# Kernel optimization log

Hardware: AMD Instinct MI355X
Metric: run time of the kernel (lower is better)

Reference implementation:

```python
import jax, jax.numpy as jnp
import numpy as np

IN, H, OUT, T, B = 132, 1024, 132, 100, 256


def setup_inputs() -> dict:
    key = jax.random.key(0)
    ks = jax.random.split(key, 16)
    s_in = 1.0 / np.sqrt(H)
    def mk(k, shape):
        return jax.random.uniform(k, shape, jnp.float32, -s_in, s_in)
    inp = {
        "real_seq": jax.random.normal(ks[0], (B, T, IN), jnp.float32),
        "W_ih1": mk(ks[1], (4 * H, IN)), "W_hh1": mk(ks[2], (4 * H, H)),
        "b_ih1": mk(ks[3], (4 * H,)),   "b_hh1": mk(ks[4], (4 * H,)),
        "W_ih2": mk(ks[5], (4 * H, H)), "W_hh2": mk(ks[6], (4 * H, H)),
        "b_ih2": mk(ks[7], (4 * H,)),   "b_hh2": mk(ks[8], (4 * H,)),
        "W_ih3": mk(ks[9], (4 * H, H)), "W_hh3": mk(ks[10], (4 * H, H)),
        "b_ih3": mk(ks[11], (4 * H,)),  "b_hh3": mk(ks[12], (4 * H,)),
        "W_dec": mk(ks[13], (OUT, H)),  "b_dec": mk(ks[14], (OUT,)),
        "condition_num": 5, "groundtruth_num": 5,
    }
    return inp


def _lstm_cell(x, h, c, W_ih, W_hh, b_ih, b_hh):
    # torch LSTMCell: gates in (i, f, g, o) order
    gates = x @ W_ih.T + b_ih + h @ W_hh.T + b_hh
    i, f, g, o = jnp.split(gates, 4, axis=-1)
    i, f, o = jax.nn.sigmoid(i), jax.nn.sigmoid(f), jax.nn.sigmoid(o)
    g = jnp.tanh(g)
    c_new = f * c + i * g
    h_new = o * jnp.tanh(c_new)
    return h_new, c_new


def reference(real_seq, W_ih1, W_hh1, b_ih1, b_hh1,
              W_ih2, W_hh2, b_ih2, b_hh2,
              W_ih3, W_hh3, b_ih3, b_hh3,
              W_dec, b_dec, condition_num, groundtruth_num):
    batch, seq_len, _ = real_seq.shape
    # static teacher-forcing schedule: [1]*gt_num + [0]*cond_num, tiled
    gt = np.ones((100, groundtruth_num)); con = np.zeros((100, condition_num))
    cond = jnp.asarray(np.concatenate((gt, con), 1).reshape(-1)[:seq_len] == 1)

    z = jnp.zeros((batch, H), jnp.float32)
    init = (z, z, z, z, z, z, jnp.zeros((batch, OUT), jnp.float32))

    def step(carry, xs):
        h0, h1, h2, c0, c1, c2, prev_out = carry
        frame, use_gt = xs
        x = jnp.where(use_gt, frame, prev_out)
        # note: lstm2/lstm3 consume the OLD h0/h1, faithful to forward_lstm
        nh0, nc0 = _lstm_cell(x,  h0, c0, W_ih1, W_hh1, b_ih1, b_hh1)
        nh1, nc1 = _lstm_cell(h0, h1, c1, W_ih2, W_hh2, b_ih2, b_hh2)
        nh2, nc2 = _lstm_cell(h1, h2, c2, W_ih3, W_hh3, b_ih3, b_hh3)
        out = nh2 @ W_dec.T + b_dec
        return (nh0, nh1, nh2, nc0, nc1, nc2, out), out

    xs = (jnp.swapaxes(real_seq, 0, 1), cond)  # [T,B,IN], [T]
    _, outs = jax.lax.scan(step, init, xs)      # outs: [T,B,OUT]
    # torch concatenates along dim 1 each step -> [B, T*OUT]
    return jnp.swapaxes(outs, 0, 1).reshape(batch, seq_len * OUT)
```

## Files before the change

kernel.cpp:

```cpp
#include <hip/hip_runtime.h>
#include <math.h>

#define B_   256
#define T_   100
#define IN_  132
#define OUT_ 132
#define H_   1024
#define BH   ((size_t)B_ * H_)
#define WSZ  ((size_t)4096 * H_)

typedef _Float16 f16;
typedef _Float16 f16x8 __attribute__((ext_vector_type(8)));
typedef float    f32x4 __attribute__((ext_vector_type(4)));

#define MFMA16(a, b, c) __builtin_amdgcn_mfma_f32_16x16x32_f16((a), (b), (c), 0, 0, 0)

#define AS1 __attribute__((address_space(1)))
#define AS3 __attribute__((address_space(3)))

__device__ __forceinline__ void gl_lds16(const void* g, void* l) {
    __builtin_amdgcn_global_load_lds((AS1 void*)g, (AS3 void*)l, 16, 0, 0);
}

__device__ __forceinline__ float sigmoidf_(float x) {
    return 1.0f / (1.0f + __expf(-x));
}
__device__ __forceinline__ float tanhf_(float x) {
    float e = __expf(2.0f * x);
    return 1.0f - 2.0f / (e + 1.0f);
}


__global__ void conv_pad(const float* __restrict__ src, f16* __restrict__ dst,
                         int src_rows, int src_k, int dst_k) {
    int k = blockIdx.x * 256 + threadIdx.x;
    int r = blockIdx.y;
    if (k >= dst_k) return;
    float v = (r < src_rows && k < src_k) ? src[(size_t)r * src_k + k] : 0.0f;
    dst[(size_t)r * dst_k + k] = (f16)v;
}

__global__ void convT_kernel(const float* __restrict__ Wd, f16* __restrict__ WdT) {
    int k = blockIdx.x * 256 + threadIdx.x;
    int m = blockIdx.y;
    if (k >= 160) return;
    float v = (k < IN_) ? Wd[(size_t)k * H_ + m] : 0.0f;
    WdT[(size_t)m * 160 + k] = (f16)v;
}

__global__ void bias_add_kernel(const float* __restrict__ a, const float* __restrict__ b,
                                float* __restrict__ dst, int n) {
    int i = blockIdx.x * 256 + threadIdx.x;
    if (i < n) dst[i] = a[i] + b[i];
}

__global__ void bfb_kernel(const float* __restrict__ Wih1, const float* __restrict__ bd,
                           float* __restrict__ bfb) {
    int j = blockIdx.x * 256 + threadIdx.x;
    if (j >= 4096) return;
    float s = 0.0f;
    for (int k = 0; k < IN_; ++k) s += Wih1[(size_t)j * IN_ + k] * bd[k];
    bfb[j] = s;
}

__global__ void zero_kernel(float* __restrict__ p, int n) {
    int i = blockIdx.x * blockDim.x + threadIdx.x;
    int st = gridDim.x * blockDim.x;
    for (; i < n; i += st) p[i] = 0.0f;
}

__global__ __launch_bounds__(256) void wfb_mfma(
    const f16* __restrict__ W0, const f16* __restrict__ WdT, f16* __restrict__ Wfb)
{
    const int m0 = blockIdx.x * 128;
    const int n0 = blockIdx.y * 128;
    const int tid  = threadIdx.x;
    const int lane = tid & 63;
    const int w    = tid >> 6;
    const int lx   = lane & 15;
    const int quad = lane >> 4;
    const int wrow = w >> 1, wcol = w & 1;

    __shared__ __align__(16) char lds[32768];

    auto stA = [&](int kt, int buf) {
        char* base = lds + buf * 16384;
#pragma unroll
        for (int i = 0; i < 2; ++i) {
            int r  = w * 32 + i * 16 + (lane >> 2);
            int sg = (lane & 3) ^ (r & 3);
            const f16* g = W0 + (size_t)(m0 + r) * 160 + kt * 32 + sg * 8;
            gl_lds16(g, base + (size_t)(w * 32 + i * 16) * 64);
        }
    };
    auto stB = [&](int kt, int buf) {
        char* base = lds + 8192 + buf * 16384;
#pragma unroll
        for (int i = 0; i < 2; ++i) {
            int r  = w * 32 + i * 16 + (lane >> 2);
            int sg = (lane & 3) ^ (r & 3);
            const f16* g = WdT + (size_t)(n0 + r) * 160 + kt * 32 + sg * 8;
            gl_lds16(g, base + (size_t)(w * 32 + i * 16) * 64);
        }
    };

    f32x4 acc[4][4];
#pragma unroll
    for (int m = 0; m < 4; ++m)
#pragma unroll
        for (int n = 0; n < 4; ++n) acc[m][n] = (f32x4){0.f, 0.f, 0.f, 0.f};

    stA(0, 0); stB(0, 0);
    for (int kt = 0; kt < 5; ++kt) {
        __syncthreads();
        if (kt + 1 < 5) { stA(kt + 1, (kt + 1) & 1); stB(kt + 1, (kt + 1) & 1); }
        const char* bA = lds + (kt & 1) * 16384;
        const char* bB = lds + 8192 + (kt & 1) * 16384;
        f16x8 af[4], bf[4];
#pragma unroll
        for (int m = 0; m < 4; ++m) {
            int R = wrow * 64 + m * 16 + lx;
            af[m] = *(const f16x8*)(bA + R * 64 + ((quad ^ (R & 3)) * 16));
        }
#pragma unroll
        for (int n = 0; n < 4; ++n) {
            int R = wcol * 64 + n * 16 + lx;
            bf[n] = *(const f16x8*)(bB + R * 64 + ((quad ^ (R & 3)) * 16));
        }
#pragma unroll
        for (int m = 0; m < 4; ++m)
#pragma unroll
            for (int n = 0; n < 4; ++n)
                acc[m][n] = MFMA16(af[m], bf[n], acc[m][n]);
    }

#pragma unroll
    for (int m = 0; m < 4; ++m)
#pragma unroll
        for (int n = 0; n < 4; ++n)
#pragma unroll
            for (int r = 0; r < 4; ++r) {
                int row = m0 + wrow * 64 + m * 16 + quad * 4 + r;
                int col = n0 + wcol * 64 + n * 16 + lx;
                Wfb[(size_t)row * H_ + col] = (f16)acc[m][n][r];
            }
}

__global__ __launch_bounds__(256) void step_mfma(
    const float* __restrict__ seq,
    const f16* __restrict__ hfb,
    const f16* __restrict__ h2old,
    const f16* __restrict__ h01c,
    f16* __restrict__ h01n,
    f16* __restrict__ h2out,
    float* __restrict__ c_st,
    const f16* __restrict__ W0,
    const f16* __restrict__ Wb,
    const f16* __restrict__ Wfb,
    const float* __restrict__ bias_comb,
    const float* __restrict__ bfb,
    const int* __restrict__ cnum, const int* __restrict__ gnum,
    int t)
{
    const int j0   = blockIdx.x * 32;
    const int mb   = blockIdx.y;
    const int l    = blockIdx.z;
    const int tid  = threadIdx.x;
    const int lane = tid & 63;
    const int w    = tid >> 6;
    const int lx   = lane & 15;
    const int quad = lane >> 4;
    const int wrow = w >> 1, wcol = w & 1;

    __shared__ __align__(16) char lds[24576];

    bool use_gt = false, seqmode = false;
    int n0 = 32, ldk0 = H_;
    const f16 *Ap0 = nullptr, *Wp0 = nullptr;
    if (l == 0) {
        int cn = cnum[0], gn = gnum[0];
        use_gt = (t % (cn + gn)) < gn;
        if (use_gt)      { seqmode = true; Wp0 = W0; ldk0 = 160; n0 = 5; }
        else if (t == 0) { n0 = 0; }
        else             { Ap0 = hfb; Wp0 = Wfb; }
    } else if (l == 1) { Ap0 = h01c;      Wp0 = Wb + 1 * WSZ; }
    else               { Ap0 = h01c + BH; Wp0 = Wb + 3 * WSZ; }
    const f16* Ap1 = (l == 0) ? h01c : (l == 1) ? (h01c + BH) : h2old;
    const f16* Wp1 = Wb + (size_t)((l == 0) ? 0 : (l == 1) ? 2 : 4) * WSZ;
    const int ntot = n0 + 32;

    auto stA = [&](const f16* Ap, int kk, int buf) {
        char* base = lds + buf * 12288 + w * 1024;
        int row = w * 16 + (lane >> 2);
        int sg  = (lane & 3) ^ (row & 3);
        const f16* g = Ap + (size_t)(mb * 64 + row) * H_ + kk * 32 + sg * 8;
        gl_lds16(g, base);
    };
    auto stAseq = [&](int kk, int buf) {
        char* base = lds + buf * 12288;
        int rl = tid >> 2, sl = tid & 3;
        int sg = sl ^ (rl & 3);
        int b  = mb * 64 + rl;
        f16x8 vv;
#pragma unroll
        for (int e = 0; e < 8; ++e) {
            int k = kk * 32 + sg * 8 + e;
            float v = (k < IN_) ? seq[((size_t)b * T_ + t) * IN_ + k] : 0.0f;
            vv[e] = (f16)v;
        }
        *(f16x8*)(base + rl * 64 + sl * 16) = vv;
    };
    auto stB = [&](const f16* Wp, size_t ldk, int kk, int buf) {
        char* base = lds + 4096 + buf * 12288;
#pragma unroll
        for (int i = 0; i < 2; ++i) {
            int c    = w * 32 + i * 16 + (lane >> 2);
            int sg   = (lane & 3) ^ (c & 3);
            int gate = (c >> 4) & 3;
            int jj   = (c & 15) + (c >> 6) * 16;
            const f16* g = Wp + (size_t)(gate * H_ + j0 + jj) * ldk + kk * 32 + sg * 8;
            gl_lds16(g, base + (size_t)(w * 32 + i * 16) * 64);
        }
    };
    auto stage = [&](int kt, int buf) {
        if (kt < n0) {
            if (seqmode) stAseq(kt, buf); else stA(Ap0, kt, buf);
            stB(Wp0, (size_t)ldk0, kt, buf);
        } else {
            stA(Ap1, kt - n0, buf);
            stB(Wp1, (size_t)H_, kt - n0, buf);
        }
    };

    f32x4 acc[2][4];
#pragma unroll
    for (int m = 0; m < 2; ++m)
#pragma unroll
        for (int n = 0; n < 4; ++n) acc[m][n] = (f32x4){0.f, 0.f, 0.f, 0.f};

    stage(0, 0);
    for (int kt = 0; kt < ntot; ++kt) {
        __syncthreads();
        if (kt + 1 < ntot) stage(kt + 1, (kt + 1) & 1);
        const char* bA = lds + (kt & 1) * 12288;
        const char* bB = lds + 4096 + (kt & 1) * 12288;
        f16x8 af[2], bf[4];
#pragma unroll
        for (int m = 0; m < 2; ++m) {
            int R = wrow * 32 + m * 16 + lx;
            af[m] = *(const f16x8*)(bA + R * 64 + ((quad ^ (R & 3)) * 16));
        }
#pragma unroll
        for (int n = 0; n < 4; ++n) {
            int R = wcol * 64 + n * 16 + lx;
            bf[n] = *(const f16x8*)(bB + R * 64 + ((quad ^ (R & 3)) * 16));
        }
#pragma unroll
        for (int m = 0; m < 2; ++m)
#pragma unroll
            for (int n = 0; n < 4; ++n)
                acc[m][n] = MFMA16(af[m], bf[n], acc[m][n]);
    }

    const int j = j0 + wcol * 16 + lx;
    const float* bc = bias_comb + l * 4096;
    const bool addfb = (l == 0 && !use_gt && t > 0);
    float bi  = bc[j]        + (addfb ? bfb[j]        : 0.f);
    float bff = bc[1024 + j] + (addfb ? bfb[1024 + j] : 0.f);
    float bg  = bc[2048 + j] + (addfb ? bfb[2048 + j] : 0.f);
    float bo  = bc[3072 + j] + (addfb ? bfb[3072 + j] : 0.f);
#pragma unroll
    for (int m = 0; m < 2; ++m) {
#pragma unroll
        for (int r = 0; r < 4; ++r) {
            int b = mb * 64 + wrow * 32 + m * 16 + quad * 4 + r;
            float gi = acc[m][0][r] + bi;
            float gf = acc[m][1][r] + bff;
            float gg = acc[m][2][r] + bg;
            float go = acc[m][3][r] + bo;
            size_t ix = ((size_t)l * B_ + b) * H_ + j;
            float cn = sigmoidf_(gf) * c_st[ix] + sigmoidf_(gi) * tanhf_(gg);
            c_st[ix] = cn;
            float hv = sigmoidf_(go) * tanhf_(cn);
            if (l == 2) h2out[(size_t)b * H_ + j] = (f16)hv;
            else        h01n[(size_t)l * BH + (size_t)b * H_ + j] = (f16)hv;
        }
    }
}

__global__ __launch_bounds__(256) void decode_mfma(
    const f16* __restrict__ hist,
    const f16* __restrict__ Wd16,
    const float* __restrict__ bd,
    float* __restrict__ dout)
{
    const int r0  = blockIdx.x * 128;
    const int nb0 = blockIdx.y * 32;
    const int tid  = threadIdx.x;
    const int lane = tid & 63;
    const int w    = tid >> 6;
    const int lx   = lane & 15;
    const int quad = lane >> 4;

    __shared__ __align__(16) char lds[20480];

    auto stA = [&](int kt, int buf) {
        char* base = lds + buf * 10240;
#pragma unroll
        for (int i = 0; i < 2; ++i) {
            int r  = w * 32 + i * 16 + (lane >> 2);
            int sg = (lane & 3) ^ (r & 3);
            const f16* g = hist + (size_t)(r0 + r) * H_ + kt * 32 + sg * 8;
            gl_lds16(g, base + (size_t)(w * 32 + i * 16) * 64);
        }
    };
    auto stB = [&](int kt, int buf) {
        char* base = lds + 8192 + buf * 10240;
        if (w < 2) {
            int r  = w * 16 + (lane >> 2);
            int sg = (lane & 3) ^ (r & 3);
            const f16* g = Wd16 + (size_t)(nb0 + r) * H_ + kt * 32 + sg * 8;
            gl_lds16(g, base + (size_t)(w * 16) * 64);
        }
    };

    f32x4 acc[2][2];
#pragma unroll
    for (int m = 0; m < 2; ++m)
#pragma unroll
        for (int n = 0; n < 2; ++n) acc[m][n] = (f32x4){0.f, 0.f, 0.f, 0.f};

    stA(0, 0); stB(0, 0);
    for (int kt = 0; kt < 32; ++kt) {
        __syncthreads();
        if (kt + 1 < 32) { stA(kt + 1, (kt + 1) & 1); stB(kt + 1, (kt + 1) & 1); }
        const char* bA = lds + (kt & 1) * 10240;
        const char* bB = lds + 8192 + (kt & 1) * 10240;
        f16x8 af[2], bf[2];
#pragma unroll
        for (int m = 0; m < 2; ++m) {
            int R = w * 32 + m * 16 + lx;
            af[m] = *(const f16x8*)(bA + R * 64 + ((quad ^ (R & 3)) * 16));
        }
#pragma unroll
        for (int n = 0; n < 2; ++n) {
            int R = n * 16 + lx;
            bf[n] = *(const f16x8*)(bB + R * 64 + ((quad ^ (R & 3)) * 16));
        }
#pragma unroll
        for (int m = 0; m < 2; ++m)
#pragma unroll
            for (int n = 0; n < 2; ++n)
                acc[m][n] = MFMA16(af[m], bf[n], acc[m][n]);
    }

#pragma unroll
    for (int n = 0; n < 2; ++n) {
        int nn = nb0 + n * 16 + lx;
        if (nn < OUT_) {
            float bv = bd[nn];
#pragma unroll
            for (int m = 0; m < 2; ++m)
#pragma unroll
                for (int r = 0; r < 4; ++r) {
                    int row = r0 + w * 32 + m * 16 + quad * 4 + r;
                    int tt = row >> 8, b = row & 255;
                    dout[(size_t)b * (T_ * OUT_) + (size_t)tt * OUT_ + nn] = acc[m][n][r] + bv;
                }
        }
    }
}


extern "C" void kernel_launch(void* const* d_in, const int* in_sizes, int n_in,
                              void* d_out, int out_size, void* d_ws, size_t ws_size,
                              hipStream_t stream) {
    const float* seq  = (const float*)d_in[0];
    const float* Wih1 = (const float*)d_in[1];
    const float* Whh1 = (const float*)d_in[2];
    const float* bih1 = (const float*)d_in[3];
    const float* bhh1 = (const float*)d_in[4];
    const float* Wih2 = (const float*)d_in[5];
    const float* Whh2 = (const float*)d_in[6];
    const float* bih2 = (const float*)d_in[7];
    const float* bhh2 = (const float*)d_in[8];
    const float* Wih3 = (const float*)d_in[9];
    const float* Whh3 = (const float*)d_in[10];
    const float* bih3 = (const float*)d_in[11];
    const float* bhh3 = (const float*)d_in[12];
    const float* Wd   = (const float*)d_in[13];
    const float* bd   = (const float*)d_in[14];
    const int*   cnum = (const int*)d_in[15];
    const int*   gnum = (const int*)d_in[16];

    char* p = (char*)d_ws;
    f16*  W0   = (f16*)p;  p += (size_t)4096 * 160 * 2;
    f16*  Wb   = (f16*)p;  p += (size_t)5 * 4096 * 1024 * 2;
    f16*  Wd16 = (f16*)p;  p += (size_t)160 * 1024 * 2;
    f16*  WdT  = (f16*)p;  p += (size_t)1024 * 160 * 2;
    f16*  Wfb  = (f16*)p;  p += (size_t)4096 * 1024 * 2;
    float* bias_comb = (float*)p; p += (size_t)3 * 4096 * 4;
    float* bfb = (float*)p; p += (size_t)4096 * 4;
    f16*  hist = (f16*)p;  p += (size_t)100 * BH * 2;
    f16*  h01a = (f16*)p;  p += (size_t)2 * BH * 2;
    f16*  h01b = (f16*)p;  p += (size_t)2 * BH * 2;
    float* c_st = (float*)p; p += (size_t)3 * BH * 4;
    const int zero_floats = (int)(((size_t)4 * BH * 2 + (size_t)3 * BH * 4) / 4);

    conv_pad<<<dim3(1, 4096), 256, 0, stream>>>(Wih1, W0, 4096, IN_, 160);
    conv_pad<<<dim3(4, 4096), 256, 0, stream>>>(Whh1, Wb + 0 * WSZ, 4096, H_, H_);
    conv_pad<<<dim3(4, 4096), 256, 0, stream>>>(Wih2, Wb + 1 * WSZ, 4096, H_, H_);
    conv_pad<<<dim3(4, 4096), 256, 0, stream>>>(Whh2, Wb + 2 * WSZ, 4096, H_, H_);
    conv_pad<<<dim3(4, 4096), 256, 0, stream>>>(Wih3, Wb + 3 * WSZ, 4096, H_, H_);
    conv_pad<<<dim3(4, 4096), 256, 0, stream>>>(Whh3, Wb + 4 * WSZ, 4096, H_, H_);
    conv_pad<<<dim3(4, 160), 256, 0, stream>>>(Wd, Wd16, OUT_, H_, H_);
    convT_kernel<<<dim3(1, 1024), 256, 0, stream>>>(Wd, WdT);
    bias_add_kernel<<<16, 256, 0, stream>>>(bih1, bhh1, bias_comb + 0 * 4096, 4096);
    bias_add_kernel<<<16, 256, 0, stream>>>(bih2, bhh2, bias_comb + 1 * 4096, 4096);
    bias_add_kernel<<<16, 256, 0, stream>>>(bih3, bhh3, bias_comb + 2 * 4096, 4096);
    bfb_kernel<<<16, 256, 0, stream>>>(Wih1, bd, bfb);
    wfb_mfma<<<dim3(32, 8), 256, 0, stream>>>(W0, WdT, Wfb);
    zero_kernel<<<512, 256, 0, stream>>>((float*)h01a, zero_floats);

    f16 *hc = h01a, *hn = h01b;
    for (int t = 0; t < T_; ++t) {
        const f16* hfb   = (t > 0) ? (hist + (size_t)(t - 1) * BH) : hc;
        const f16* h2old = (t > 0) ? (hist + (size_t)(t - 1) * BH) : hc;
        step_mfma<<<dim3(32, 4, 3), 256, 0, stream>>>(
            seq, hfb, h2old, hc, hn, hist + (size_t)t * BH, c_st,
            W0, Wb, Wfb, bias_comb, bfb, cnum, gnum, t);
        f16* tmp = hc; hc = hn; hn = tmp;
    }

    decode_mfma<<<dim3(200, 5), 256, 0, stream>>>(hist, Wd16, bd, (float*)d_out);
}
```

Baseline: 3.387 ms.

## Deepen step kernel K-loop to 4-stage async LDS pipeline and pre-pad sequence to fp16

The per-timestep LSTM GEMM kernel moves from a double-buffered LDS loop to a four-buffer ring that keeps three tiles of async global-to-LDS loads in flight. It waits on explicit vmcnt values and issues MFMAs at raised wave priority. The input sequence is converted once to padded fp16 in a prologue kernel, so the teacher-forced path can use the same async load path instead of per-thread fp32 gathers. The goal is to hide global memory latency in the latency-bound small-grid step kernel. The cost is doubled LDS use, which may lower occupancy, plus hand-counted waitcnt logic that must match the number of loads issued per stage.

Result: faster. 3.151 ms (-7.0%).

```diff
diff --git a/kernel.cpp b/kernel.cpp
--- a/kernel.cpp
+++ b/kernel.cpp
@@ -38,6 +38,14 @@
     if (k >= dst_k) return;
     float v = (r < src_rows && k < src_k) ? src[(size_t)r * src_k + k] : 0.0f;
     dst[(size_t)r * dst_k + k] = (f16)v;
+}
+
+__global__ void seq_pad(const float* __restrict__ src, f16* __restrict__ dst) {
+    int k  = threadIdx.x;
+    int bt = blockIdx.y;
+    if (k >= 160) return;
+    float v = (k < IN_) ? src[(size_t)bt * IN_ + k] : 0.0f;
+    dst[(size_t)bt * 160 + k] = (f16)v;
 }
 
 __global__ void convT_kernel(const float* __restrict__ Wd, f16* __restrict__ WdT) {
@@ -147,7 +155,7 @@
 }
 
 __global__ __launch_bounds__(256) void step_mfma(
-    const float* __restrict__ seq,
+    const f16* __restrict__ seq16,
     const f16* __restrict__ hfb,
     const f16* __restrict__ h2old,
     const f16* __restrict__ h01c,
@@ -172,15 +180,17 @@
     const int quad = lane >> 4;
     const int wrow = w >> 1, wcol = w & 1;
 
-    __shared__ __align__(16) char lds[24576];
-
-    bool use_gt = false, seqmode = false;
-    int n0 = 32, ldk0 = H_;
+    __shared__ __align__(16) char lds[49152];
+
+    bool use_gt = false;
+    int n0 = 32;
+    size_t ldA0 = H_, ldB0 = H_;
     const f16 *Ap0 = nullptr, *Wp0 = nullptr;
     if (l == 0) {
         int cn = cnum[0], gn = gnum[0];
         use_gt = (t % (cn + gn)) < gn;
-        if (use_gt)      { seqmode = true; Wp0 = W0; ldk0 = 160; n0 = 5; }
+        if (use_gt)      { Ap0 = seq16 + (size_t)t * 160; ldA0 = (size_t)T_ * 160;
+                           Wp0 = W0; ldB0 = 160; n0 = 5; }
         else if (t == 0) { n0 = 0; }
         else             { Ap0 = hfb; Wp0 = Wfb; }
     } else if (l == 1) { Ap0 = h01c;      Wp0 = Wb + 1 * WSZ; }
@@ -189,29 +199,15 @@
     const f16* Wp1 = Wb + (size_t)((l == 0) ? 0 : (l == 1) ? 2 : 4) * WSZ;
     const int ntot = n0 + 32;
 
-    auto stA = [&](const f16* Ap, int kk, int buf) {
+    auto stA = [&](const f16* Ap, size_t ldA, int kk, int buf) {
         char* base = lds + buf * 12288 + w * 1024;
         int row = w * 16 + (lane >> 2);
         int sg  = (lane & 3) ^ (row & 3);
-        const f16* g = Ap + (size_t)(mb * 64 + row) * H_ + kk * 32 + sg * 8;
+        const f16* g = Ap + (size_t)(mb * 64 + row) * ldA + kk * 32 + sg * 8;
         gl_lds16(g, base);
     };
-    auto stAseq = [&](int kk, int buf) {
-        char* base = lds + buf * 12288;
-        int rl = tid >> 2, sl = tid & 3;
-        int sg = sl ^ (rl & 3);
-        int b  = mb * 64 + rl;
-        f16x8 vv;
-#pragma unroll
-        for (int e = 0; e < 8; ++e) {
-            int k = kk * 32 + sg * 8 + e;
-            float v = (k < IN_) ? seq[((size_t)b * T_ + t) * IN_ + k] : 0.0f;
-            vv[e] = (f16)v;
-        }
-        *(f16x8*)(base + rl * 64 + sl * 16) = vv;
-    };
     auto stB = [&](const f16* Wp, size_t ldk, int kk, int buf) {
-        char* base = lds + 4096 + buf * 12288;
+        char* base = lds + buf * 12288 + 4096;
 #pragma unroll
         for (int i = 0; i < 2; ++i) {
             int c    = w * 32 + i * 16 + (lane >> 2);
@@ -224,10 +220,10 @@
     };
     auto stage = [&](int kt, int buf) {
         if (kt < n0) {
-            if (seqmode) stAseq(kt, buf); else stA(Ap0, kt, buf);
-            stB(Wp0, (size_t)ldk0, kt, buf);
+            stA(Ap0, ldA0, kt, buf);
+            stB(Wp0, ldB0, kt, buf);
         } else {
-            stA(Ap1, kt - n0, buf);
+            stA(Ap1, (size_t)H_, kt - n0, buf);
             stB(Wp1, (size_t)H_, kt - n0, buf);
         }
     };
@@ -239,11 +235,17 @@
         for (int n = 0; n < 4; ++n) acc[m][n] = (f32x4){0.f, 0.f, 0.f, 0.f};
 
     stage(0, 0);
+    stage(1, 1);
+    stage(2, 2);
+
     for (int kt = 0; kt < ntot; ++kt) {
-        __syncthreads();
-        if (kt + 1 < ntot) stage(kt + 1, (kt + 1) & 1);
-        const char* bA = lds + (kt & 1) * 12288;
-        const char* bB = lds + 4096 + (kt & 1) * 12288;
+        if (kt < ntot - 2)       asm volatile("s_waitcnt vmcnt(6)" ::: "memory");
+        else if (kt == ntot - 2) asm volatile("s_waitcnt vmcnt(3)" ::: "memory");
+        else                     asm volatile("s_waitcnt vmcnt(0)" ::: "memory");
+        __builtin_amdgcn_s_barrier();
+
+        const char* bA = lds + (kt & 3) * 12288;
+        const char* bB = bA + 4096;
         f16x8 af[2], bf[4];
 #pragma unroll
         for (int m = 0; m < 2; ++m) {
@@ -255,11 +257,19 @@
             int R = wcol * 64 + n * 16 + lx;
             bf[n] = *(const f16x8*)(bB + R * 64 + ((quad ^ (R & 3)) * 16));
         }
+        asm volatile("s_waitcnt lgkmcnt(0)" ::: "memory");
+        __builtin_amdgcn_sched_barrier(0);
+        __builtin_amdgcn_s_barrier();
+
+        if (kt + 3 < ntot) stage(kt + 3, (kt + 3) & 3);
+
+        __builtin_amdgcn_s_setprio(1);
 #pragma unroll
         for (int m = 0; m < 2; ++m)
 #pragma unroll
             for (int n = 0; n < 4; ++n)
                 acc[m][n] = MFMA16(af[m], bf[n], acc[m][n]);
+        __builtin_amdgcn_s_setprio(0);
     }
 
     const int j = j0 + wcol * 16 + lx;
@@ -405,6 +415,7 @@
     f16*  h01a = (f16*)p;  p += (size_t)2 * BH * 2;
     f16*  h01b = (f16*)p;  p += (size_t)2 * BH * 2;
     float* c_st = (float*)p; p += (size_t)3 * BH * 4;
+    f16*  seq16 = (f16*)p; p += (size_t)B_ * T_ * 160 * 2;
     const int zero_floats = (int)(((size_t)4 * BH * 2 + (size_t)3 * BH * 4) / 4);
 
     conv_pad<<<dim3(1, 4096), 256, 0, stream>>>(Wih1, W0, 4096, IN_, 160);
@@ -415,6 +426,7 @@
     conv_pad<<<dim3(4, 4096), 256, 0, stream>>>(Whh3, Wb + 4 * WSZ, 4096, H_, H_);
     conv_pad<<<dim3(4, 160), 256, 0, stream>>>(Wd, Wd16, OUT_, H_, H_);
     convT_kernel<<<dim3(1, 1024), 256, 0, stream>>>(Wd, WdT);
+    seq_pad<<<dim3(1, B_ * T_), 256, 0, stream>>>(seq, seq16);
     bias_add_kernel<<<16, 256, 0, stream>>>(bih1, bhh1, bias_comb + 0 * 4096, 4096);
     bias_add_kernel<<<16, 256, 0, stream>>>(bih2, bhh2, bias_comb + 1 * 4096, 4096);
     bias_add_kernel<<<16, 256, 0, stream>>>(bih3, bhh3, bias_comb + 2 * 4096, 4096);
@@ -427,7 +439,7 @@
         const f16* hfb   = (t > 0) ? (hist + (size_t)(t - 1) * BH) : hc;
         const f16* h2old = (t > 0) ? (hist + (size_t)(t - 1) * BH) : hc;
         step_mfma<<<dim3(32, 4, 3), 256, 0, stream>>>(
-            seq, hfb, h2old, hc, hn, hist + (size_t)t * BH, c_st,
+            seq16, hfb, h2old, hc, hn, hist + (size_t)t * BH, c_st,
             W0, Wb, Wfb, bias_comb, bfb, cnum, gnum, t);
         f16* tmp = hc; hc = hn; hn = tmp;
     }
```
